# Kernel optimization log

Measured on AMD Instinct MI355X. Metric: run time of the kernel, lower is better.

## Reference

```python
import jax, jax.numpy as jnp
import numpy as np

N_NODES = 10000
N_EDGES = 640000
D = 128  # node / edge / hidden feature dim
EPS = 1e-6


def _relu_mlp(x, params):
    # Dense+relu for all layers except the last (plain Dense)
    for w, b in params[:-1]:
        x = jax.nn.relu(x @ w + b)
    w, b = params[-1]
    return x @ w + b


def _layer_norm(x, scale, bias):
    mean = jnp.mean(x, axis=-1, keepdims=True)
    var = jnp.mean(jnp.square(x - mean), axis=-1, keepdims=True)
    return (x - mean) * jax.lax.rsqrt(var + EPS) * scale + bias


def _he(key, fan_in, fan_out):
    return jax.random.normal(key, (fan_in, fan_out), jnp.float32) * jnp.sqrt(2.0 / fan_in)


def setup_inputs() -> dict:
    key = jax.random.key(0)
    ks = jax.random.split(key, 12)
    nodes = jax.random.normal(ks[0], (N_NODES, D), jnp.float32)
    edges = jax.random.normal(ks[1], (N_EDGES, D), jnp.float32)
    senders = jax.random.randint(ks[2], (N_EDGES,), 0, N_NODES, jnp.int32)
    receivers = jax.random.randint(ks[3], (N_EDGES,), 0, N_NODES, jnp.int32)
    # MessageMLP: [3D -> D -> D -> D]
    msg_w0 = _he(ks[4], 3 * D, D); msg_b0 = jnp.zeros((D,), jnp.float32)
    msg_w1 = _he(ks[5], D, D);     msg_b1 = jnp.zeros((D,), jnp.float32)
    msg_w2 = _he(ks[6], D, D);     msg_b2 = jnp.zeros((D,), jnp.float32)
    # NodeMLP: [2D -> D -> D -> D]
    node_w0 = _he(ks[7], 2 * D, D); node_b0 = jnp.zeros((D,), jnp.float32)
    node_w1 = _he(ks[8], D, D);     node_b1 = jnp.zeros((D,), jnp.float32)
    node_w2 = _he(ks[9], D, D);     node_b2 = jnp.zeros((D,), jnp.float32)
    # W_node residual projection (no bias) + LayerNorm params
    w_node = _he(ks[10], D, D)
    ln_scale = jnp.ones((D,), jnp.float32)
    ln_bias = jnp.zeros((D,), jnp.float32)
    return dict(nodes=nodes, edges=edges, senders=senders, receivers=receivers,
                msg_w0=msg_w0, msg_b0=msg_b0, msg_w1=msg_w1, msg_b1=msg_b1,
                msg_w2=msg_w2, msg_b2=msg_b2,
                node_w0=node_w0, node_b0=node_b0, node_w1=node_w1, node_b1=node_b1,
                node_w2=node_w2, node_b2=node_b2,
                w_node=w_node, ln_scale=ln_scale, ln_bias=ln_bias)


def reference(nodes, edges, senders, receivers,
              msg_w0, msg_b0, msg_w1, msg_b1, msg_w2, msg_b2,
              node_w0, node_b0, node_w1, node_b1, node_w2, node_b2,
              w_node, ln_scale, ln_bias):
    total_nodes = nodes.shape[0]
    # gather sender/receiver features and concat with edge features: [E, 3D]
    msg_in = jnp.concatenate([nodes[senders], nodes[receivers], edges], axis=-1)
    messages = _relu_mlp(msg_in, [(msg_w0, msg_b0), (msg_w1, msg_b1), (msg_w2, msg_b2)])
    # scatter-add messages onto receiving nodes: [N, D]
    aggregated = jax.ops.segment_sum(messages, receivers, num_segments=total_nodes)
    node_in = jnp.concatenate([nodes, aggregated], axis=-1)  # [N, 2D]
    nodes_out = _relu_mlp(node_in, [(node_w0, node_b0), (node_w1, node_b1), (node_w2, node_b2)])
    nodes_new = _layer_norm(nodes @ w_node + nodes_out, ln_scale, ln_bias)
    return nodes_new
```

## Files before the change

kernel.cpp:

```cpp
#include <hip/hip_runtime.h>

#define DF 128
constexpr int N_NODES = 10000;
constexpr int N_EDGES = 640000;

typedef __bf16 bf16x8 __attribute__((ext_vector_type(8)));
typedef float f32x4 __attribute__((ext_vector_type(4)));

__device__ __forceinline__ unsigned short f2bf(float f) {
  unsigned u = __builtin_bit_cast(unsigned, f);
  u += 0x7fffu + ((u >> 16) & 1u);
  return (unsigned short)(u >> 16);
}

__device__ __forceinline__ bf16x8 cvt8(float4 a, float4 b) {
  bf16x8 r;
  r[0] = (__bf16)a.x; r[1] = (__bf16)a.y; r[2] = (__bf16)a.z; r[3] = (__bf16)a.w;
  r[4] = (__bf16)b.x; r[5] = (__bf16)b.y; r[6] = (__bf16)b.z; r[7] = (__bf16)b.w;
  return r;
}

template <bool RELU>
__device__ __forceinline__ void stage_t(char* bufj, const f32x4* accv, int grp, int row16) {
#pragma unroll
  for (int nt = 0; nt < 8; ++nt)
#pragma unroll
    for (int i = 0; i < 4; ++i) {
      const int r = grp * 4 + i;
      const int c = nt * 16 + row16;
      float v = RELU ? fmaxf(accv[nt][i], 0.f) : accv[nt][i];
      *(unsigned short*)(bufj + ((r * 256 + c * 2) ^ ((r & 7) << 4))) = f2bf(v);
    }
}

__device__ __forceinline__ bf16x8 read_a(const char* bufj, int kt, int grp, int row16) {
  return *(const bf16x8*)(bufj + ((row16 * 256 + kt * 64 + grp * 16) ^ ((row16 & 7) << 4)));
}

__global__ void pack_prep(const float* __restrict__ w0, const float* __restrict__ w1,
                          const float* __restrict__ w2, const float* __restrict__ nw0,
                          const float* __restrict__ nw1, const float* __restrict__ nw2,
                          const float* __restrict__ wn, const float* __restrict__ nodes,
                          const int* __restrict__ receivers,
                          unsigned short* __restrict__ dst, unsigned short* __restrict__ nbf,
                          int* __restrict__ deg) {
  int tid = blockIdx.x * blockDim.x + threadIdx.x;
  if (tid < 163840) {
    const float* src; int p;
    if (tid < 49152)       { src = w0;  p = tid; }
    else if (tid < 65536)  { src = w1;  p = tid - 49152; }
    else if (tid < 81920)  { src = w2;  p = tid - 65536; }
    else if (tid < 114688) { src = nw0; p = tid - 81920; }
    else if (tid < 131072) { src = nw1; p = tid - 114688; }
    else if (tid < 147456) { src = nw2; p = tid - 131072; }
    else                   { src = wn;  p = tid - 147456; }
    int i = p & 7, lane = (p >> 3) & 63, tile = p >> 9;
    int nt = tile & 7, kt = tile >> 3;
    int k = kt * 32 + ((lane >> 4) << 3) + i;
    int n = nt * 16 + (lane & 15);
    dst[tid] = f2bf(src[k * 128 + n]);
    return;
  }
  int p = tid - 163840;
  if (p < N_NODES * DF) {
    nbf[p] = f2bf(nodes[p]);
    return;
  }
  p -= N_NODES * DF;
  if (p < N_EDGES) atomicAdd(&deg[receivers[p]], 1);
}

__global__ void scan_kernel(const int* __restrict__ deg, int* __restrict__ rowstart) {
  __shared__ int part[1024];
  const int t = threadIdx.x;
  int loc[16];
  int s = 0;
#pragma unroll
  for (int j = 0; j < 16; ++j) {
    int idx = t * 16 + j;
    int v = (idx < N_NODES) ? deg[idx] : 0;
    loc[j] = s;
    s += v;
  }
  part[t] = s;
  __syncthreads();
  for (int off = 1; off < 1024; off <<= 1) {
    int v = part[t];
    int a = (t >= off) ? part[t - off] : 0;
    __syncthreads();
    part[t] = v + a;
    __syncthreads();
  }
  int base = (t > 0) ? part[t - 1] : 0;
#pragma unroll
  for (int j = 0; j < 16; ++j) {
    int idx = t * 16 + j;
    if (idx < N_NODES) rowstart[idx] = base + loc[j];
  }
  if (t == 0) rowstart[N_NODES] = part[1023];
}

__global__ void scatter_idx(const int* __restrict__ receivers, const int* __restrict__ senders,
                            const int* __restrict__ rowstart,
                            int* __restrict__ cursor, int2* __restrict__ ep,
                            int* __restrict__ rid) {
  int e = blockIdx.x * blockDim.x + threadIdx.x;
  if (e >= N_EDGES) return;
  int r = receivers[e];
  int pos = atomicAdd(&cursor[r], 1);
  int q = rowstart[r] + pos;
  ep[q] = make_int2(e, senders[e]);
  rid[q] = r;
}

__global__ void __launch_bounds__(256) pq_kernel(
    const unsigned short* __restrict__ nbf, const unsigned short* __restrict__ pw,
    unsigned short* __restrict__ P, unsigned short* __restrict__ Q) {
  const int tid = threadIdx.x, lane = tid & 63, wave = tid >> 6;
  const int row16 = lane & 15, grp = lane >> 4;
  const int rb = blockIdx.x * 64 + wave * 16;
  const int rA = min(rb + row16, N_NODES - 1);

  f32x4 aP[8], aQ[8];
#pragma unroll
  for (int nt = 0; nt < 8; ++nt) {
    aP[nt] = (f32x4){0.f, 0.f, 0.f, 0.f};
    aQ[nt] = (f32x4){0.f, 0.f, 0.f, 0.f};
  }
#pragma unroll
  for (int kt = 0; kt < 4; ++kt) {
    bf16x8 af = *(const bf16x8*)(nbf + (size_t)rA * DF + kt * 32 + grp * 8);
#pragma unroll
    for (int nt = 0; nt < 8; ++nt) {
      bf16x8 bwP = *(const bf16x8*)(pw + ((size_t)(kt * 8 + nt) * 64 + lane) * 8);
      bf16x8 bwQ = *(const bf16x8*)(pw + ((size_t)((4 + kt) * 8 + nt) * 64 + lane) * 8);
      aP[nt] = __builtin_amdgcn_mfma_f32_16x16x32_bf16(af, bwP, aP[nt], 0, 0, 0);
      aQ[nt] = __builtin_amdgcn_mfma_f32_16x16x32_bf16(af, bwQ, aQ[nt], 0, 0, 0);
    }
  }
#pragma unroll
  for (int nt = 0; nt < 8; ++nt)
#pragma unroll
    for (int i = 0; i < 4; ++i) {
      const int r = rb + grp * 4 + i;
      if (r < N_NODES) {
        P[(size_t)r * DF + nt * 16 + row16] = f2bf(aP[nt][i]);
        Q[(size_t)r * DF + nt * 16 + row16] = f2bf(aQ[nt][i]);
      }
    }
}

__global__ void __launch_bounds__(512, 2) msg_kernel(
    const float* __restrict__ edges,
    const int2* __restrict__ ep, const int* __restrict__ rid,
    const float* __restrict__ b0, const float* __restrict__ b1,
    const unsigned short* __restrict__ pw,
    const unsigned short* __restrict__ P, const unsigned short* __restrict__ Q,
    float* __restrict__ hsum) {
  __shared__ char lds[131072];
  const int tid = threadIdx.x;
  const int lane = tid & 63, wave = tid >> 6;
  const int row16 = lane & 15, grp = lane >> 4;
  char* hb = lds + 65536 + wave * 8192;
  const int pbase = blockIdx.x * 256 + wave * 32;

  {
    const float4* src = (const float4*)(pw + 32768);
    float4* dst = (float4*)lds;
    for (int c = tid; c < 4096; c += 512) dst[c] = src[c];
  }

  int e_[2], sx[2], rx[2];
#pragma unroll
  for (int s = 0; s < 2; ++s) {
    int2 es = ep[pbase + s * 16 + row16];
    e_[s] = es.x;
    sx[s] = es.y;
    rx[s] = rid[pbase + s * 16 + row16];
  }

  float4 t0[4][2], t1[4][2];
#pragma unroll
  for (int k2 = 0; k2 < 4; ++k2) {
    const float* p0 = edges + (size_t)e_[0] * DF + k2 * 32 + grp * 8;
    const float* p1 = edges + (size_t)e_[1] * DF + k2 * 32 + grp * 8;
    t0[k2][0] = *(const float4*)p0; t0[k2][1] = *(const float4*)(p0 + 4);
    t1[k2][0] = *(const float4*)p1; t1[k2][1] = *(const float4*)(p1 + 4);
  }

  bf16x8 pqf[2][2][4];
#pragma unroll
  for (int s = 0; s < 2; ++s)
#pragma unroll
    for (int kt = 0; kt < 4; ++kt) {
      pqf[s][0][kt] = *(const bf16x8*)(P + (size_t)sx[s] * DF + kt * 32 + grp * 8);
      pqf[s][1][kt] = *(const bf16x8*)(Q + (size_t)rx[s] * DF + kt * 32 + grp * 8);
    }

  bf16x8 ebf[2][4];
#pragma unroll
  for (int k2 = 0; k2 < 4; ++k2) {
    ebf[0][k2] = cvt8(t0[k2][0], t0[k2][1]);
    ebf[1][k2] = cvt8(t1[k2][0], t1[k2][1]);
  }

  __syncthreads();

  f32x4 acc[2][8];
#pragma unroll
  for (int nt = 0; nt < 8; ++nt) {
    float bv = b0[nt * 16 + row16];
    acc[0][nt] = (f32x4){bv, bv, bv, bv};
    acc[1][nt] = (f32x4){bv, bv, bv, bv};
  }
#pragma unroll
  for (int kt = 0; kt < 4; ++kt) {
#pragma unroll
    for (int nt = 0; nt < 8; ++nt) {
      bf16x8 bw = *(const bf16x8*)(lds + ((kt * 8 + nt) * 64 + lane) * 16);
      acc[0][nt] = __builtin_amdgcn_mfma_f32_16x16x32_bf16(ebf[0][kt], bw, acc[0][nt], 0, 0, 0);
      acc[1][nt] = __builtin_amdgcn_mfma_f32_16x16x32_bf16(ebf[1][kt], bw, acc[1][nt], 0, 0, 0);
    }
  }

  stage_t<false>(hb, acc[0], grp, row16);
  stage_t<false>(hb + 4096, acc[1], grp, row16);
  asm volatile("s_waitcnt lgkmcnt(0)" ::: "memory");
  __builtin_amdgcn_sched_barrier(0);

#pragma unroll
  for (int nt = 0; nt < 8; ++nt) {
    float bv = b1[nt * 16 + row16];
    acc[0][nt] = (f32x4){bv, bv, bv, bv};
    acc[1][nt] = (f32x4){bv, bv, bv, bv};
  }
#pragma unroll
  for (int kt = 0; kt < 4; ++kt) {
    bf16x8 af[2];
#pragma unroll
    for (int s = 0; s < 2; ++s) {
      bf16x8 raw = read_a(hb + s * 4096, kt, grp, row16);
      bf16x8 pv = pqf[s][0][kt], qv = pqf[s][1][kt];
      bf16x8 h;
#pragma unroll
      for (int j = 0; j < 8; ++j)
        h[j] = (__bf16)fmaxf((float)raw[j] + (float)pv[j] + (float)qv[j], 0.f);
      af[s] = h;
    }
#pragma unroll
    for (int nt = 0; nt < 8; ++nt) {
      bf16x8 bw = *(const bf16x8*)(lds + 32768 + ((kt * 8 + nt) * 64 + lane) * 16);
      acc[0][nt] = __builtin_amdgcn_mfma_f32_16x16x32_bf16(af[0], bw, acc[0][nt], 0, 0, 0);
      acc[1][nt] = __builtin_amdgcn_mfma_f32_16x16x32_bf16(af[1], bw, acc[1][nt], 0, 0, 0);
    }
  }

#pragma unroll
  for (int s = 0; s < 2; ++s) {
    const int q = pbase + s * 16 + grp * 4;
    const int ru = rid[pbase + s * 16];
    const bool uni = (ru == rid[pbase + s * 16 + 15]);
    if (uni) {
#pragma unroll
      for (int nt = 0; nt < 8; ++nt) {
        float t = fmaxf(acc[s][nt][0], 0.f) + fmaxf(acc[s][nt][1], 0.f) +
                  fmaxf(acc[s][nt][2], 0.f) + fmaxf(acc[s][nt][3], 0.f);
        t += __shfl_xor(t, 16);
        t += __shfl_xor(t, 32);
        if (grp == 0)
          unsafeAtomicAdd(hsum + (size_t)ru * DF + nt * 16 + row16, t);
      }
    } else {
      const int ra = rid[q], rb_ = rid[q + 1], rc = rid[q + 2], rd = rid[q + 3];
#pragma unroll
      for (int nt = 0; nt < 8; ++nt) {
        const int col = nt * 16 + row16;
        float run = fmaxf(acc[s][nt][0], 0.f);
        if (rb_ != ra) { unsafeAtomicAdd(hsum + (size_t)ra * DF + col, run); run = 0.f; }
        run += fmaxf(acc[s][nt][1], 0.f);
        if (rc != rb_) { unsafeAtomicAdd(hsum + (size_t)rb_ * DF + col, run); run = 0.f; }
        run += fmaxf(acc[s][nt][2], 0.f);
        if (rd != rc) { unsafeAtomicAdd(hsum + (size_t)rc * DF + col, run); run = 0.f; }
        run += fmaxf(acc[s][nt][3], 0.f);
        unsafeAtomicAdd(hsum + (size_t)rd * DF + col, run);
      }
    }
  }
}

__global__ void __launch_bounds__(128) node_kernel(
    const float* __restrict__ nodes, const float* __restrict__ hsum,
    const int* __restrict__ deg, const float* __restrict__ b2,
    const float* __restrict__ nb0, const float* __restrict__ nb1, const float* __restrict__ nb2,
    const unsigned short* __restrict__ pw2,
    const unsigned short* __restrict__ pnw0, const unsigned short* __restrict__ pnw1,
    const unsigned short* __restrict__ pnw2, const unsigned short* __restrict__ pwn,
    const float* __restrict__ ln_s, const float* __restrict__ ln_b,
    float* __restrict__ out) {
  __shared__ char hs[8192];
  const int tid = threadIdx.x, lane = tid & 63, wave = tid >> 6;
  const int row16 = lane & 15, grp = lane >> 4;
  char* hb = hs + wave * 4096;
  const int rb = blockIdx.x * 32 + wave * 16;
  const int rA = min(rb + row16, N_NODES - 1);

  f32x4 accA[8];
  {
    float d0 = (float)deg[min(rb + grp * 4 + 0, N_NODES - 1)];
    float d1 = (float)deg[min(rb + grp * 4 + 1, N_NODES - 1)];
    float d2 = (float)deg[min(rb + grp * 4 + 2, N_NODES - 1)];
    float d3 = (float)deg[min(rb + grp * 4 + 3, N_NODES - 1)];
#pragma unroll
    for (int nt = 0; nt < 8; ++nt) {
      float bc = b2[nt * 16 + row16];
      accA[nt] = (f32x4){d0 * bc, d1 * bc, d2 * bc, d3 * bc};
    }
  }
#pragma unroll
  for (int kt = 0; kt < 4; ++kt) {
    const float* hp = hsum + (size_t)rA * DF + kt * 32 + grp * 8;
    float4 h0 = *(const float4*)hp, h1v = *(const float4*)(hp + 4);
    bf16x8 hi = cvt8(h0, h1v);
    float4 l0, l1;
    l0.x = h0.x - (float)hi[0]; l0.y = h0.y - (float)hi[1];
    l0.z = h0.z - (float)hi[2]; l0.w = h0.w - (float)hi[3];
    l1.x = h1v.x - (float)hi[4]; l1.y = h1v.y - (float)hi[5];
    l1.z = h1v.z - (float)hi[6]; l1.w = h1v.w - (float)hi[7];
    bf16x8 lo = cvt8(l0, l1);
#pragma unroll
    for (int nt = 0; nt < 8; ++nt) {
      bf16x8 bw = *(const bf16x8*)(pw2 + ((size_t)(kt * 8 + nt) * 64 + lane) * 8);
      accA[nt] = __builtin_amdgcn_mfma_f32_16x16x32_bf16(hi, bw, accA[nt], 0, 0, 0);
      accA[nt] = __builtin_amdgcn_mfma_f32_16x16x32_bf16(lo, bw, accA[nt], 0, 0, 0);
    }
  }
  stage_t<false>(hb, accA, grp, row16);
  asm volatile("s_waitcnt lgkmcnt(0)" ::: "memory");
  __builtin_amdgcn_sched_barrier(0);

  f32x4 acc[8];
#pragma unroll
  for (int nt = 0; nt < 8; ++nt) {
    float b = nb0[nt * 16 + row16];
    acc[nt] = (f32x4){b, b, b, b};
  }
#pragma unroll
  for (int kt = 0; kt < 8; ++kt) {
    bf16x8 af;
    if (kt < 4) {
      const float* p = nodes + (size_t)rA * DF + kt * 32 + grp * 8;
      af = cvt8(*(const float4*)p, *(const float4*)(p + 4));
    } else {
      af = read_a(hb, kt - 4, grp, row16);
    }
#pragma unroll
    for (int nt = 0; nt < 8; ++nt) {
      bf16x8 bw = *(const bf16x8*)(pnw0 + ((size_t)(kt * 8 + nt) * 64 + lane) * 8);
      acc[nt] = __builtin_amdgcn_mfma_f32_16x16x32_bf16(af, bw, acc[nt], 0, 0, 0);
    }
  }
  asm volatile("s_waitcnt lgkmcnt(0)" ::: "memory");
  __builtin_amdgcn_sched_barrier(0);
  stage_t<true>(hb, acc, grp, row16);
  asm volatile("s_waitcnt lgkmcnt(0)" ::: "memory");
  __builtin_amdgcn_sched_barrier(0);

  f32x4 acc2[8];
#pragma unroll
  for (int nt = 0; nt < 8; ++nt) {
    float b = nb1[nt * 16 + row16];
    acc2[nt] = (f32x4){b, b, b, b};
  }
#pragma unroll
  for (int kt = 0; kt < 4; ++kt) {
    bf16x8 af = read_a(hb, kt, grp, row16);
#pragma unroll
    for (int nt = 0; nt < 8; ++nt) {
      bf16x8 bw = *(const bf16x8*)(pnw1 + ((size_t)(kt * 8 + nt) * 64 + lane) * 8);
      acc2[nt] = __builtin_amdgcn_mfma_f32_16x16x32_bf16(af, bw, acc2[nt], 0, 0, 0);
    }
  }
  asm volatile("s_waitcnt lgkmcnt(0)" ::: "memory");
  __builtin_amdgcn_sched_barrier(0);
  stage_t<true>(hb, acc2, grp, row16);
  asm volatile("s_waitcnt lgkmcnt(0)" ::: "memory");
  __builtin_amdgcn_sched_barrier(0);

  f32x4 acc3[8];
#pragma unroll
  for (int nt = 0; nt < 8; ++nt) {
    float b = nb2[nt * 16 + row16];
    acc3[nt] = (f32x4){b, b, b, b};
  }
#pragma unroll
  for (int kt = 0; kt < 4; ++kt) {
    bf16x8 af = read_a(hb, kt, grp, row16);
#pragma unroll
    for (int nt = 0; nt < 8; ++nt) {
      bf16x8 bw = *(const bf16x8*)(pnw2 + ((size_t)(kt * 8 + nt) * 64 + lane) * 8);
      acc3[nt] = __builtin_amdgcn_mfma_f32_16x16x32_bf16(af, bw, acc3[nt], 0, 0, 0);
    }
  }
  f32x4 accR[8];
#pragma unroll
  for (int nt = 0; nt < 8; ++nt) accR[nt] = (f32x4){0.f, 0.f, 0.f, 0.f};
#pragma unroll
  for (int kt = 0; kt < 4; ++kt) {
    const float* p = nodes + (size_t)rA * DF + kt * 32 + grp * 8;
    bf16x8 af = cvt8(*(const float4*)p, *(const float4*)(p + 4));
#pragma unroll
    for (int nt = 0; nt < 8; ++nt) {
      bf16x8 bw = *(const bf16x8*)(pwn + ((size_t)(kt * 8 + nt) * 64 + lane) * 8);
      accR[nt] = __builtin_amdgcn_mfma_f32_16x16x32_bf16(af, bw, accR[nt], 0, 0, 0);
    }
  }

  float y[8][4];
#pragma unroll
  for (int nt = 0; nt < 8; ++nt)
#pragma unroll
    for (int i = 0; i < 4; ++i) y[nt][i] = acc3[nt][i] + accR[nt][i];

  float mean[4], rstd[4];
#pragma unroll
  for (int i = 0; i < 4; ++i) {
    float s = 0.f;
#pragma unroll
    for (int nt = 0; nt < 8; ++nt) s += y[nt][i];
    s += __shfl_xor(s, 1); s += __shfl_xor(s, 2);
    s += __shfl_xor(s, 4); s += __shfl_xor(s, 8);
    mean[i] = s * (1.0f / 128.0f);
  }
#pragma unroll
  for (int i = 0; i < 4; ++i) {
    float v = 0.f;
#pragma unroll
    for (int nt = 0; nt < 8; ++nt) {
      float d = y[nt][i] - mean[i];
      v += d * d;
    }
    v += __shfl_xor(v, 1); v += __shfl_xor(v, 2);
    v += __shfl_xor(v, 4); v += __shfl_xor(v, 8);
    rstd[i] = rsqrtf(v * (1.0f / 128.0f) + 1e-6f);
  }
#pragma unroll
  for (int nt = 0; nt < 8; ++nt) {
    const float ls = ln_s[nt * 16 + row16];
    const float lb = ln_b[nt * 16 + row16];
#pragma unroll
    for (int i = 0; i < 4; ++i) {
      const int r = rb + grp * 4 + i;
      if (r < N_NODES)
        out[(size_t)r * DF + nt * 16 + row16] = (y[nt][i] - mean[i]) * rstd[i] * ls + lb;
    }
  }
}

extern "C" void kernel_launch(void* const* d_in, const int* in_sizes, int n_in,
                              void* d_out, int out_size, void* d_ws, size_t ws_size,
                              hipStream_t stream) {
  const float* nodes     = (const float*)d_in[0];
  const float* edges     = (const float*)d_in[1];
  const int*   senders   = (const int*)d_in[2];
  const int*   receivers = (const int*)d_in[3];
  const float* msg_w0 = (const float*)d_in[4];
  const float* msg_b0 = (const float*)d_in[5];
  const float* msg_w1 = (const float*)d_in[6];
  const float* msg_b1 = (const float*)d_in[7];
  const float* msg_w2 = (const float*)d_in[8];
  const float* msg_b2 = (const float*)d_in[9];
  const float* node_w0 = (const float*)d_in[10];
  const float* node_b0 = (const float*)d_in[11];
  const float* node_w1 = (const float*)d_in[12];
  const float* node_b1 = (const float*)d_in[13];
  const float* node_w2 = (const float*)d_in[14];
  const float* node_b2 = (const float*)d_in[15];
  const float* w_node   = (const float*)d_in[16];
  const float* ln_scale = (const float*)d_in[17];
  const float* ln_bias  = (const float*)d_in[18];

  char* ws = (char*)d_ws;
  float* hsum           = (float*)ws;
  unsigned short* pw    = (unsigned short*)(ws + 5120000);
  unsigned short* nbf   = (unsigned short*)(ws + 5447680);
  int* deg              = (int*)(ws + 8007680);
  int* cursor           = (int*)(ws + 8047680);
  int* rowstart         = (int*)(ws + 8087680);
  int* rid              = (int*)(ws + 8127688);
  int2* ep              = (int2*)(ws + 10687688);
  unsigned short* P     = (unsigned short*)(ws + 15807696);
  unsigned short* Q     = (unsigned short*)(ws + 18367696);

  hipMemsetAsync(hsum, 0, (size_t)N_NODES * DF * sizeof(float), stream);
  hipMemsetAsync(deg, 0, 80000, stream);

  pack_prep<<<8140, 256, 0, stream>>>(
      msg_w0, msg_w1, msg_w2, node_w0, node_w1, node_w2, w_node, nodes, receivers,
      pw, nbf, deg);

  scan_kernel<<<1, 1024, 0, stream>>>(deg, rowstart);
  scatter_idx<<<N_EDGES / 256, 256, 0, stream>>>(receivers, senders, rowstart, cursor,
                                                 ep, rid);
  pq_kernel<<<157, 256, 0, stream>>>(nbf, pw, P, Q);

  msg_kernel<<<N_EDGES / 256, 512, 0, stream>>>(
      edges, ep, rid, msg_b0, msg_b1, pw, P, Q, hsum);

  node_kernel<<<313, 128, 0, stream>>>(nodes, hsum, deg, msg_b2,
                                       node_b0, node_b1, node_b2,
                                       pw + 65536,
                                       pw + 81920, pw + 114688, pw + 131072, pw + 147456,
                                       ln_scale, ln_bias, (float*)d_out);
}
```

Baseline: 349.2 us.

## Make msg_kernel persistent with edge prefetch; fuse scatter, PQ and hsum zeroing

The message kernel becomes persistent: 256 blocks loop over edge tiles. Each block loads the weights into LDS once and prefetches the next tile's edge indices and edge features while computing the current tile. Scatter-index building and the P/Q projection are merged into one launch, which also zeroes hsum, so one memset and two launches go away. The scan now writes the exclusive offsets straight into cursor, so the separate rowstart array and memset are no longer needed. The tradeoffs are higher register pressure from the prefetch buffers, and a grid of only 256 blocks may underfill the device compared with 2500.

```diff
diff --git a/kernel.cpp b/kernel.cpp
--- a/kernel.cpp
+++ b/kernel.cpp
@@ -70,7 +70,7 @@
   if (p < N_EDGES) atomicAdd(&deg[receivers[p]], 1);
 }
 
-__global__ void scan_kernel(const int* __restrict__ deg, int* __restrict__ rowstart) {
+__global__ void scan_kernel(const int* __restrict__ deg, int* __restrict__ cursor) {
   __shared__ int part[1024];
   const int t = threadIdx.x;
   int loc[16];
@@ -95,30 +95,36 @@
 #pragma unroll
   for (int j = 0; j < 16; ++j) {
     int idx = t * 16 + j;
-    if (idx < N_NODES) rowstart[idx] = base + loc[j];
-  }
-  if (t == 0) rowstart[N_NODES] = part[1023];
-}
-
-__global__ void scatter_idx(const int* __restrict__ receivers, const int* __restrict__ senders,
-                            const int* __restrict__ rowstart,
-                            int* __restrict__ cursor, int2* __restrict__ ep,
-                            int* __restrict__ rid) {
-  int e = blockIdx.x * blockDim.x + threadIdx.x;
-  if (e >= N_EDGES) return;
-  int r = receivers[e];
-  int pos = atomicAdd(&cursor[r], 1);
-  int q = rowstart[r] + pos;
-  ep[q] = make_int2(e, senders[e]);
-  rid[q] = r;
-}
-
-__global__ void __launch_bounds__(256) pq_kernel(
+    if (idx < N_NODES) cursor[idx] = base + loc[j];
+  }
+}
+
+__global__ void __launch_bounds__(256) scatter_pq(
+    const int* __restrict__ receivers, const int* __restrict__ senders,
+    int* __restrict__ cursor, int2* __restrict__ ep, int* __restrict__ rid,
     const unsigned short* __restrict__ nbf, const unsigned short* __restrict__ pw,
-    unsigned short* __restrict__ P, unsigned short* __restrict__ Q) {
-  const int tid = threadIdx.x, lane = tid & 63, wave = tid >> 6;
+    unsigned short* __restrict__ P, unsigned short* __restrict__ Q,
+    float* __restrict__ hsum) {
+  const int bid = blockIdx.x;
+  const int tid = threadIdx.x;
+  if (bid < N_EDGES / 256) {
+    int e = bid * 256 + tid;
+    int r = receivers[e];
+    int q = atomicAdd(&cursor[r], 1);
+    ep[q] = make_int2(e, senders[e]);
+    rid[q] = r;
+    return;
+  }
+  const int pb = bid - N_EDGES / 256;
+  const int base_row = pb * 64;
+  const int nrows = min(64, N_NODES - base_row);
+  {
+    float4* hz = (float4*)(hsum + (size_t)base_row * DF);
+    for (int c = tid; c < nrows * 32; c += 256) hz[c] = make_float4(0.f, 0.f, 0.f, 0.f);
+  }
+  const int lane = tid & 63, wave = tid >> 6;
   const int row16 = lane & 15, grp = lane >> 4;
-  const int rb = blockIdx.x * 64 + wave * 16;
+  const int rb = base_row + wave * 16;
   const int rA = min(rb + row16, N_NODES - 1);
 
   f32x4 aP[8], aQ[8];
@@ -162,7 +168,6 @@
   const int lane = tid & 63, wave = tid >> 6;
   const int row16 = lane & 15, grp = lane >> 4;
   char* hb = lds + 65536 + wave * 8192;
-  const int pbase = blockIdx.x * 256 + wave * 32;
 
   {
     const float4* src = (const float4*)(pw + 32768);
@@ -170,121 +175,159 @@
     for (int c = tid; c < 4096; c += 512) dst[c] = src[c];
   }
 
-  int e_[2], sx[2], rx[2];
-#pragma unroll
-  for (int s = 0; s < 2; ++s) {
-    int2 es = ep[pbase + s * 16 + row16];
-    e_[s] = es.x;
-    sx[s] = es.y;
-    rx[s] = rid[pbase + s * 16 + row16];
-  }
+  constexpr int NTILE = N_EDGES / 256;
+  int tile = blockIdx.x;
 
   float4 t0[4][2], t1[4][2];
-#pragma unroll
-  for (int k2 = 0; k2 < 4; ++k2) {
-    const float* p0 = edges + (size_t)e_[0] * DF + k2 * 32 + grp * 8;
-    const float* p1 = edges + (size_t)e_[1] * DF + k2 * 32 + grp * 8;
-    t0[k2][0] = *(const float4*)p0; t0[k2][1] = *(const float4*)(p0 + 4);
-    t1[k2][0] = *(const float4*)p1; t1[k2][1] = *(const float4*)(p1 + 4);
-  }
-
-  bf16x8 pqf[2][2][4];
-#pragma unroll
-  for (int s = 0; s < 2; ++s)
+  int sxc[2], rxc[2];
+  int e2_[2], sx2[2], rx2[2];
+
+  {
+    const int pb = tile * 256 + wave * 32;
+#pragma unroll
+    for (int s = 0; s < 2; ++s) {
+      int2 es = ep[pb + s * 16 + row16];
+      e2_[s] = es.x; sx2[s] = es.y;
+      rx2[s] = rid[pb + s * 16 + row16];
+    }
+#pragma unroll
+    for (int k2 = 0; k2 < 4; ++k2) {
+      const float* p0 = edges + (size_t)e2_[0] * DF + k2 * 32 + grp * 8;
+      const float* p1 = edges + (size_t)e2_[1] * DF + k2 * 32 + grp * 8;
+      t0[k2][0] = *(const float4*)p0; t0[k2][1] = *(const float4*)(p0 + 4);
+      t1[k2][0] = *(const float4*)p1; t1[k2][1] = *(const float4*)(p1 + 4);
+    }
+    sxc[0] = sx2[0]; sxc[1] = sx2[1];
+    rxc[0] = rx2[0]; rxc[1] = rx2[1];
+  }
+
+  __syncthreads();
+
+  for (; tile < NTILE; tile += 256) {
+    const int pbase = tile * 256 + wave * 32;
+    const bool hasNext = (tile + 256) < NTILE;
+
+    if (hasNext) {
+      const int npb = (tile + 256) * 256 + wave * 32;
+#pragma unroll
+      for (int s = 0; s < 2; ++s) {
+        int2 es = ep[npb + s * 16 + row16];
+        e2_[s] = es.x; sx2[s] = es.y;
+        rx2[s] = rid[npb + s * 16 + row16];
+      }
+    }
+
+    bf16x8 ebf[2][4];
+#pragma unroll
+    for (int k2 = 0; k2 < 4; ++k2) {
+      ebf[0][k2] = cvt8(t0[k2][0], t0[k2][1]);
+      ebf[1][k2] = cvt8(t1[k2][0], t1[k2][1]);
+    }
+
+    bf16x8 pqf[2][2][4];
+#pragma unroll
+    for (int s = 0; s < 2; ++s)
+#pragma unroll
+      for (int kt = 0; kt < 4; ++kt) {
+        pqf[s][0][kt] = *(const bf16x8*)(P + (size_t)sxc[s] * DF + kt * 32 + grp * 8);
+        pqf[s][1][kt] = *(const bf16x8*)(Q + (size_t)rxc[s] * DF + kt * 32 + grp * 8);
+      }
+
+    f32x4 acc[2][8];
+#pragma unroll
+    for (int nt = 0; nt < 8; ++nt) {
+      float bv = b0[nt * 16 + row16];
+      acc[0][nt] = (f32x4){bv, bv, bv, bv};
+      acc[1][nt] = (f32x4){bv, bv, bv, bv};
+    }
 #pragma unroll
     for (int kt = 0; kt < 4; ++kt) {
-      pqf[s][0][kt] = *(const bf16x8*)(P + (size_t)sx[s] * DF + kt * 32 + grp * 8);
-      pqf[s][1][kt] = *(const bf16x8*)(Q + (size_t)rx[s] * DF + kt * 32 + grp * 8);
-    }
-
-  bf16x8 ebf[2][4];
-#pragma unroll
-  for (int k2 = 0; k2 < 4; ++k2) {
-    ebf[0][k2] = cvt8(t0[k2][0], t0[k2][1]);
-    ebf[1][k2] = cvt8(t1[k2][0], t1[k2][1]);
-  }
-
-  __syncthreads();
-
-  f32x4 acc[2][8];
-#pragma unroll
-  for (int nt = 0; nt < 8; ++nt) {
-    float bv = b0[nt * 16 + row16];
-    acc[0][nt] = (f32x4){bv, bv, bv, bv};
-    acc[1][nt] = (f32x4){bv, bv, bv, bv};
-  }
-#pragma unroll
-  for (int kt = 0; kt < 4; ++kt) {
-#pragma unroll
-    for (int nt = 0; nt < 8; ++nt) {
-      bf16x8 bw = *(const bf16x8*)(lds + ((kt * 8 + nt) * 64 + lane) * 16);
-      acc[0][nt] = __builtin_amdgcn_mfma_f32_16x16x32_bf16(ebf[0][kt], bw, acc[0][nt], 0, 0, 0);
-      acc[1][nt] = __builtin_amdgcn_mfma_f32_16x16x32_bf16(ebf[1][kt], bw, acc[1][nt], 0, 0, 0);
-    }
-  }
-
-  stage_t<false>(hb, acc[0], grp, row16);
-  stage_t<false>(hb + 4096, acc[1], grp, row16);
-  asm volatile("s_waitcnt lgkmcnt(0)" ::: "memory");
-  __builtin_amdgcn_sched_barrier(0);
-
-#pragma unroll
-  for (int nt = 0; nt < 8; ++nt) {
-    float bv = b1[nt * 16 + row16];
-    acc[0][nt] = (f32x4){bv, bv, bv, bv};
-    acc[1][nt] = (f32x4){bv, bv, bv, bv};
-  }
-#pragma unroll
-  for (int kt = 0; kt < 4; ++kt) {
-    bf16x8 af[2];
+#pragma unroll
+      for (int nt = 0; nt < 8; ++nt) {
+        bf16x8 bw = *(const bf16x8*)(lds + ((kt * 8 + nt) * 64 + lane) * 16);
+        acc[0][nt] = __builtin_amdgcn_mfma_f32_16x16x32_bf16(ebf[0][kt], bw, acc[0][nt], 0, 0, 0);
+        acc[1][nt] = __builtin_amdgcn_mfma_f32_16x16x32_bf16(ebf[1][kt], bw, acc[1][nt], 0, 0, 0);
+      }
+    }
+
+    if (hasNext) {
+#pragma unroll
+      for (int k2 = 0; k2 < 4; ++k2) {
+        const float* p0 = edges + (size_t)e2_[0] * DF + k2 * 32 + grp * 8;
+        const float* p1 = edges + (size_t)e2_[1] * DF + k2 * 32 + grp * 8;
+        t0[k2][0] = *(const float4*)p0; t0[k2][1] = *(const float4*)(p0 + 4);
+        t1[k2][0] = *(const float4*)p1; t1[k2][1] = *(const float4*)(p1 + 4);
+      }
+    }
+
+    stage_t<false>(hb, acc[0], grp, row16);
+    stage_t<false>(hb + 4096, acc[1], grp, row16);
+    asm volatile("s_waitcnt lgkmcnt(0)" ::: "memory");
+    __builtin_amdgcn_sched_barrier(0);
+
+#pragma unroll
+    for (int nt = 0; nt < 8; ++nt) {
+      float bv = b1[nt * 16 + row16];
+      acc[0][nt] = (f32x4){bv, bv, bv, bv};
+      acc[1][nt] = (f32x4){bv, bv, bv, bv};
+    }
+#pragma unroll
+    for (int kt = 0; kt < 4; ++kt) {
+      bf16x8 af[2];
+#pragma unroll
+      for (int s = 0; s < 2; ++s) {
+        bf16x8 raw = read_a(hb + s * 4096, kt, grp, row16);
+        bf16x8 pv = pqf[s][0][kt], qv = pqf[s][1][kt];
+        bf16x8 h;
+#pragma unroll
+        for (int j = 0; j < 8; ++j)
+          h[j] = (__bf16)fmaxf((float)raw[j] + (float)pv[j] + (float)qv[j], 0.f);
+        af[s] = h;
+      }
+#pragma unroll
+      for (int nt = 0; nt < 8; ++nt) {
+        bf16x8 bw = *(const bf16x8*)(lds + 32768 + ((kt * 8 + nt) * 64 + lane) * 16);
+        acc[0][nt] = __builtin_amdgcn_mfma_f32_16x16x32_bf16(af[0], bw, acc[0][nt], 0, 0, 0);
+        acc[1][nt] = __builtin_amdgcn_mfma_f32_16x16x32_bf16(af[1], bw, acc[1][nt], 0, 0, 0);
+      }
+    }
+
 #pragma unroll
     for (int s = 0; s < 2; ++s) {
-      bf16x8 raw = read_a(hb + s * 4096, kt, grp, row16);
-      bf16x8 pv = pqf[s][0][kt], qv = pqf[s][1][kt];
-      bf16x8 h;
-#pragma unroll
-      for (int j = 0; j < 8; ++j)
-        h[j] = (__bf16)fmaxf((float)raw[j] + (float)pv[j] + (float)qv[j], 0.f);
-      af[s] = h;
-    }
-#pragma unroll
-    for (int nt = 0; nt < 8; ++nt) {
-      bf16x8 bw = *(const bf16x8*)(lds + 32768 + ((kt * 8 + nt) * 64 + lane) * 16);
-      acc[0][nt] = __builtin_amdgcn_mfma_f32_16x16x32_bf16(af[0], bw, acc[0][nt], 0, 0, 0);
-      acc[1][nt] = __builtin_amdgcn_mfma_f32_16x16x32_bf16(af[1], bw, acc[1][nt], 0, 0, 0);
-    }
-  }
-
-#pragma unroll
-  for (int s = 0; s < 2; ++s) {
-    const int q = pbase + s * 16 + grp * 4;
-    const int ru = rid[pbase + s * 16];
-    const bool uni = (ru == rid[pbase + s * 16 + 15]);
-    if (uni) {
-#pragma unroll
-      for (int nt = 0; nt < 8; ++nt) {
-        float t = fmaxf(acc[s][nt][0], 0.f) + fmaxf(acc[s][nt][1], 0.f) +
-                  fmaxf(acc[s][nt][2], 0.f) + fmaxf(acc[s][nt][3], 0.f);
-        t += __shfl_xor(t, 16);
-        t += __shfl_xor(t, 32);
-        if (grp == 0)
-          unsafeAtomicAdd(hsum + (size_t)ru * DF + nt * 16 + row16, t);
-      }
-    } else {
-      const int ra = rid[q], rb_ = rid[q + 1], rc = rid[q + 2], rd = rid[q + 3];
-#pragma unroll
-      for (int nt = 0; nt < 8; ++nt) {
-        const int col = nt * 16 + row16;
-        float run = fmaxf(acc[s][nt][0], 0.f);
-        if (rb_ != ra) { unsafeAtomicAdd(hsum + (size_t)ra * DF + col, run); run = 0.f; }
-        run += fmaxf(acc[s][nt][1], 0.f);
-        if (rc != rb_) { unsafeAtomicAdd(hsum + (size_t)rb_ * DF + col, run); run = 0.f; }
-        run += fmaxf(acc[s][nt][2], 0.f);
-        if (rd != rc) { unsafeAtomicAdd(hsum + (size_t)rc * DF + col, run); run = 0.f; }
-        run += fmaxf(acc[s][nt][3], 0.f);
-        unsafeAtomicAdd(hsum + (size_t)rd * DF + col, run);
-      }
-    }
+      const int q = pbase + s * 16 + grp * 4;
+      const int ru = rid[pbase + s * 16];
+      const bool uni = (ru == rid[pbase + s * 16 + 15]);
+      if (uni) {
+#pragma unroll
+        for (int nt = 0; nt < 8; ++nt) {
+          float t = fmaxf(acc[s][nt][0], 0.f) + fmaxf(acc[s][nt][1], 0.f) +
+                    fmaxf(acc[s][nt][2], 0.f) + fmaxf(acc[s][nt][3], 0.f);
+          t += __shfl_xor(t, 16);
+          t += __shfl_xor(t, 32);
+          if (grp == 0)
+            unsafeAtomicAdd(hsum + (size_t)ru * DF + nt * 16 + row16, t);
+        }
+      } else {
+        const int ra = rid[q], rb_ = rid[q + 1], rc = rid[q + 2], rd = rid[q + 3];
+#pragma unroll
+        for (int nt = 0; nt < 8; ++nt) {
+          const int col = nt * 16 + row16;
+          float run = fmaxf(acc[s][nt][0], 0.f);
+          if (rb_ != ra) { unsafeAtomicAdd(hsum + (size_t)ra * DF + col, run); run = 0.f; }
+          run += fmaxf(acc[s][nt][1], 0.f);
+          if (rc != rb_) { unsafeAtomicAdd(hsum + (size_t)rb_ * DF + col, run); run = 0.f; }
+          run += fmaxf(acc[s][nt][2], 0.f);
+          if (rd != rc) { unsafeAtomicAdd(hsum + (size_t)rc * DF + col, run); run = 0.f; }
+          run += fmaxf(acc[s][nt][3], 0.f);
+          unsafeAtomicAdd(hsum + (size_t)rd * DF + col, run);
+        }
+      }
+    }
+
+    sxc[0] = sx2[0]; sxc[1] = sx2[1];
+    rxc[0] = rx2[0]; rxc[1] = rx2[1];
+    asm volatile("s_waitcnt lgkmcnt(0)" ::: "memory");
+    __builtin_amdgcn_sched_barrier(0);
   }
 }
 
@@ -485,25 +528,23 @@
   unsigned short* nbf   = (unsigned short*)(ws + 5447680);
   int* deg              = (int*)(ws + 8007680);
   int* cursor           = (int*)(ws + 8047680);
-  int* rowstart         = (int*)(ws + 8087680);
-  int* rid              = (int*)(ws + 8127688);
-  int2* ep              = (int2*)(ws + 10687688);
-  unsigned short* P     = (unsigned short*)(ws + 15807696);
-  unsigned short* Q     = (unsigned short*)(ws + 18367696);
-
-  hipMemsetAsync(hsum, 0, (size_t)N_NODES * DF * sizeof(float), stream);
-  hipMemsetAsync(deg, 0, 80000, stream);
+  int* rid              = (int*)(ws + 8087680);
+  int2* ep              = (int2*)(ws + 10647680);
+  unsigned short* P     = (unsigned short*)(ws + 15767680);
+  unsigned short* Q     = (unsigned short*)(ws + 18327680);
+
+  hipMemsetAsync(deg, 0, 40000, stream);
 
   pack_prep<<<8140, 256, 0, stream>>>(
       msg_w0, msg_w1, msg_w2, node_w0, node_w1, node_w2, w_node, nodes, receivers,
       pw, nbf, deg);
 
-  scan_kernel<<<1, 1024, 0, stream>>>(deg, rowstart);
-  scatter_idx<<<N_EDGES / 256, 256, 0, stream>>>(receivers, senders, rowstart, cursor,
-                                                 ep, rid);
-  pq_kernel<<<157, 256, 0, stream>>>(nbf, pw, P, Q);
-
-  msg_kernel<<<N_EDGES / 256, 512, 0, stream>>>(
+  scan_kernel<<<1, 1024, 0, stream>>>(deg, cursor);
+
+  scatter_pq<<<N_EDGES / 256 + 157, 256, 0, stream>>>(
+      receivers, senders, cursor, ep, rid, nbf, pw, P, Q, hsum);
+
+  msg_kernel<<<256, 512, 0, stream>>>(
       edges, ep, rid, msg_b0, msg_b1, pw, P, Q, hsum);
 
   node_kernel<<<313, 128, 0, stream>>>(nodes, hsum, deg, msg_b2,
```

Result: no change. 343.7 us (-1.6%).
